# Kernel optimization log

Measured on AMD Instinct MI355X. Metric: run time of the kernel, lower is better.

## Reference

```python
import jax, jax.numpy as jnp
import numpy as np


def setup_inputs() -> dict:
    key = jax.random.key(0)
    k1, k2 = jax.random.split(key)
    x = jax.random.normal(k1, (2048, 512, 7, 7), dtype=jnp.float32)   # backbone feature map [B, C, H, W]
    db = jax.random.normal(k2, (50000, 512), dtype=jnp.float32)       # gallery embeddings [N, D]
    return {"x": x, "db": db}


def reference(x, db):
    # backbone output is a 4D feature map -> global average pool over H, W
    emb = x.mean(axis=(2, 3))                      # [B, 512]; width == 512 so no pad/slice
    # torch.cdist(emb, db, p=2) via ||a||^2 - 2ab + ||b||^2 decomposition
    a2 = jnp.sum(emb * emb, axis=1, keepdims=True)         # [B, 1]
    b2 = jnp.sum(db * db, axis=1)                          # [N]
    d2 = a2 - 2.0 * (emb @ db.T) + b2[None, :]             # [B, N]
    dist = jnp.sqrt(jnp.maximum(d2, 0.0))
    min_dist = jnp.min(dist, axis=1)                       # [B]
    min_idx = jnp.argmin(dist, axis=1)                     # [B] int
    return min_dist, min_idx
```

## Files before the change

kernel.cpp:

```cpp
#include <hip/hip_runtime.h>
#include <math.h>
#include <stdint.h>

#define D      512
#define K2T    1056
#define HW     49
#define BM     128
#define BN     128
#define BK     32
#define NSWEEP 4
#define KSTEPS 33
#define TTOT   (NSWEEP * KSTEPS)

typedef __attribute__((ext_vector_type(8))) _Float16 f16x8;
typedef __attribute__((ext_vector_type(4))) float f32x4;
typedef __attribute__((address_space(3))) uint32_t lds_t;
typedef const __attribute__((address_space(1))) uint32_t glb_t;

__global__ __launch_bounds__(256) void gap_split_kernel(const float* __restrict__ x,
                                                        _Float16* __restrict__ emb2) {
    __shared__ float g[256 * HW];
    const int tid = threadIdx.x;
    const float4* x4 = (const float4*)x + (size_t)blockIdx.x * (256 * HW / 4);
    float4* g4 = (float4*)g;
#pragma unroll
    for (int i = 0; i < 12; ++i) {
        g4[tid + i * 256] = x4[tid + i * 256];
    }
    if (tid < 64) g4[tid + 3072] = x4[tid + 3072];
    __syncthreads();
    const float* p = g + tid * HW;
    float s = 0.f;
#pragma unroll
    for (int j = 0; j < HW; ++j) s += p[j];
    s *= (1.f / 49.f);
    _Float16 hi = (_Float16)s;
    _Float16 lo = (_Float16)(s - (float)hi);
    int r = blockIdx.x * 256 + tid;
    int m = r >> 9, c = r & 511;
    emb2[(size_t)m * K2T + c]       = hi;
    emb2[(size_t)m * K2T + 512 + c] = lo;
}

__global__ void finishA_kernel(_Float16* __restrict__ emb2, int M) {
    int row = blockIdx.x * 4 + (threadIdx.x >> 6);
    if (row >= M) return;
    int lane = threadIdx.x & 63;
    _Float16* p = emb2 + (size_t)row * K2T;
    f16x8 h = *(const f16x8*)(p + lane * 8);
    f16x8 l = *(const f16x8*)(p + 512 + lane * 8);
    float s = 0.f;
#pragma unroll
    for (int i = 0; i < 8; ++i) { float v = (float)h[i] + (float)l[i]; s = fmaf(v, v, s); }
#pragma unroll
    for (int m2 = 32; m2; m2 >>= 1) s += __shfl_xor(s, m2, 64);
    if (lane == 0) {
        _Float16 a2h = (_Float16)s;
        _Float16 a2l = (_Float16)(s - (float)a2h);
        _Float16 one = (_Float16)1.f, z0 = (_Float16)0.f;
        f16x8 t0 = {one, one, a2h, a2l, z0, z0, z0, z0};
        f16x8 z  = {z0, z0, z0, z0, z0, z0, z0, z0};
        *(f16x8*)(p + 1024) = t0;
        *(f16x8*)(p + 1032) = z;
        *(f16x8*)(p + 1040) = z;
        *(f16x8*)(p + 1048) = z;
    }
}

__global__ void split_db_kernel(const float* __restrict__ db,
                                _Float16* __restrict__ db2, int N, int N2) {
    int row = blockIdx.x * 4 + (threadIdx.x >> 6);
    if (row >= N2) return;
    int lane = threadIdx.x & 63;
    _Float16* q = db2 + (size_t)row * K2T;
    _Float16 z0 = (_Float16)0.f;
    f16x8 z = {z0, z0, z0, z0, z0, z0, z0, z0};
    if (row < N) {
        const float* p = db + (size_t)row * D + lane * 8;
        float4 v0 = *(const float4*)p;
        float4 v1 = *(const float4*)(p + 4);
        float vv[8] = {v0.x, v0.y, v0.z, v0.w, v1.x, v1.y, v1.z, v1.w};
        f16x8 h, l;
        float s = 0.f;
#pragma unroll
        for (int i = 0; i < 8; ++i) {
            float v = vv[i];
            s = fmaf(v, v, s);
            float wv = -2.f * v;
            _Float16 hh = (_Float16)wv;
            h[i] = hh;
            l[i] = (_Float16)(wv - (float)hh);
        }
        *(f16x8*)(q + lane * 8)       = h;
        *(f16x8*)(q + 512 + lane * 8) = l;
#pragma unroll
        for (int m2 = 32; m2; m2 >>= 1) s += __shfl_xor(s, m2, 64);
        if (lane == 0) {
            _Float16 b2h = (_Float16)s;
            _Float16 b2l = (_Float16)(s - (float)b2h);
            _Float16 one = (_Float16)1.f;
            f16x8 t0 = {b2h, b2l, one, one, z0, z0, z0, z0};
            *(f16x8*)(q + 1024) = t0;
            *(f16x8*)(q + 1032) = z;
            *(f16x8*)(q + 1040) = z;
            *(f16x8*)(q + 1048) = z;
        }
    } else {
        *(f16x8*)(q + lane * 8)       = z;
        *(f16x8*)(q + 512 + lane * 8) = z;
        if (lane < 4) *(f16x8*)(q + 1024 + lane * 8) = z;
    }
}

__global__ void init_keys_kernel(unsigned long long* __restrict__ keys, int M) {
    int b = blockIdx.x * blockDim.x + threadIdx.x;
    if (b < M) keys[b] = ~0ull;
}

__global__ __launch_bounds__(256) void dist_kernel(
        const _Float16* __restrict__ A2, const _Float16* __restrict__ B2,
        unsigned long long* __restrict__ keys, int N, int nXcdChunk)
{
    __shared__ _Float16 lds[3 * 8192];
    const int tid  = threadIdx.x;
    const int lane = tid & 63;
    const int w    = tid >> 6;
    const int wr   = w >> 1, wc = w & 1;
    const int l15  = lane & 15, lg = lane >> 4;

    const int bb   = blockIdx.x;
    const int swz  = (bb & 7) * nXcdChunk + (bb >> 3);
    const int mBase = (swz & 15) * BM;
    const long long nSuperBase = (long long)(swz >> 4) * (BN * NSWEEP);

    const int o0 = w * 1024 + lane * 16;

    auto STAGE = [&](unsigned bufByte, int tt) {
        const int k0 = (tt % KSTEPS) * BK;
        const long long nB = nSuperBase + (long long)(tt / KSTEPS) * BN;
#pragma unroll
        for (int q = 0; q < 2; ++q) {
            const int o = o0 + q * 4096;
            const int row = o >> 6;
            const int slot = (o >> 4) & 3;
            const int cb = ((slot ^ ((row >> 1) & 3)) << 4);
            const char* ga = (const char*)A2 + ((size_t)(mBase + row) * K2T + k0) * 2 + cb;
            const char* gb = (const char*)B2 + ((size_t)(nB + row) * K2T + k0) * 2 + cb;
            char* la = (char*)lds + bufByte + q * 4096 + w * 1024;
            __builtin_amdgcn_global_load_lds((glb_t*)ga, (lds_t*)la, 16, 0, 0);
            __builtin_amdgcn_global_load_lds((glb_t*)gb, (lds_t*)(la + 8192), 16, 0, 0);
        }
    };

    unsigned long long key[4][4];
#pragma unroll
    for (int mF = 0; mF < 4; ++mF)
#pragma unroll
        for (int r = 0; r < 4; ++r) key[mF][r] = ~0ull;

    f32x4 acc[4][4];
#pragma unroll
    for (int mF = 0; mF < 4; ++mF)
#pragma unroll
        for (int nF = 0; nF < 4; ++nF) acc[mF][nF] = (f32x4){0.f, 0.f, 0.f, 0.f};

    STAGE(0, 0);
    STAGE(16384, 1);
    unsigned bufR = 0, bufN = 16384, bufP = 32768;

    const int sw = (lg ^ ((l15 >> 1) & 3)) * 8;

    for (int t = 0; t < TTOT; ++t) {
        if (t < TTOT - 1) asm volatile("s_waitcnt vmcnt(4)" ::: "memory");
        else              asm volatile("s_waitcnt vmcnt(0)" ::: "memory");
        __builtin_amdgcn_s_barrier();

        const _Float16* As = (const _Float16*)((const char*)lds + bufR);
        const _Float16* Bs = As + 4096;
        f16x8 af[4], bf[4];
#pragma unroll
        for (int mF = 0; mF < 4; ++mF)
            af[mF] = *(const f16x8*)(As + (wr * 64 + mF * 16 + l15) * BK + sw);
#pragma unroll
        for (int nF = 0; nF < 4; ++nF)
            bf[nF] = *(const f16x8*)(Bs + (wc * 64 + nF * 16 + l15) * BK + sw);

        if (t + 2 < TTOT) STAGE(bufP, t + 2);

        __builtin_amdgcn_s_setprio(1);
#pragma unroll
        for (int mF = 0; mF < 4; ++mF)
#pragma unroll
            for (int nF = 0; nF < 4; ++nF)
                acc[mF][nF] = __builtin_amdgcn_mfma_f32_16x16x32_f16(
                    af[mF], bf[nF], acc[mF][nF], 0, 0, 0);
        __builtin_amdgcn_s_setprio(0);

        if (t % KSTEPS == KSTEPS - 1) {
            const long long nBase = nSuperBase + (long long)(t / KSTEPS) * BN;
#pragma unroll
            for (int nF = 0; nF < 4; ++nF) {
                const long long g = nBase + wc * 64 + nF * 16 + l15;
                if (g < N) {
#pragma unroll
                    for (int mF = 0; mF < 4; ++mF)
#pragma unroll
                        for (int r = 0; r < 4; ++r) {
                            float d2 = fmaxf(acc[mF][nF][r], 0.f);
                            unsigned long long kk =
                                ((unsigned long long)__float_as_uint(d2) << 32) |
                                (unsigned long long)(unsigned)g;
                            key[mF][r] = key[mF][r] < kk ? key[mF][r] : kk;
                        }
                }
            }
#pragma unroll
            for (int mF = 0; mF < 4; ++mF)
#pragma unroll
                for (int nF = 0; nF < 4; ++nF) acc[mF][nF] = (f32x4){0.f, 0.f, 0.f, 0.f};
        }

        unsigned tmp = bufR; bufR = bufN; bufN = bufP; bufP = tmp;
    }

#pragma unroll
    for (int mF = 0; mF < 4; ++mF)
#pragma unroll
        for (int r = 0; r < 4; ++r) {
            unsigned long long k = key[mF][r];
#pragma unroll
            for (int m2 = 1; m2 < 16; m2 <<= 1) {
                unsigned long long o = __shfl_xor(k, m2, 16);
                k = k < o ? k : o;
            }
            if (l15 == 0)
                atomicMin(&keys[mBase + wr * 64 + mF * 16 + lg * 4 + r], k);
        }
}

__global__ void finalize_kernel(const unsigned long long* __restrict__ keys,
                                float* __restrict__ out_dist, float* __restrict__ out_idx, int M) {
    int b = blockIdx.x * blockDim.x + threadIdx.x;
    if (b >= M) return;
    unsigned long long k = keys[b];
    float d2 = __uint_as_float((unsigned)(k >> 32));
    out_dist[b] = sqrtf(fmaxf(d2, 0.f));
    out_idx[b]  = (float)(unsigned)(k & 0xffffffffu);
}

extern "C" void kernel_launch(void* const* d_in, const int* in_sizes, int n_in,
                              void* d_out, int out_size, void* d_ws, size_t ws_size,
                              hipStream_t stream) {
    const float* x  = (const float*)d_in[0];
    const float* db = (const float*)d_in[1];
    float* out = (float*)d_out;

    const int M  = in_sizes[0] / (D * HW);
    const int N  = in_sizes[1] / D;
    const int nTiles  = (N + BN - 1) / BN;
    const int nSupers = (nTiles + NSWEEP - 1) / NSWEEP;
    const int N2 = nSupers * NSWEEP * BN;
    const int mTiles = M / BM;
    const int nBlocks = nSupers * mTiles;
    const int nXcdChunk = nBlocks / 8;

    char* ws = (char*)d_ws;
    _Float16* emb2 = (_Float16*)ws;
    _Float16* db2  = emb2 + (size_t)M * K2T;
    unsigned long long* keys =
        (unsigned long long*)(((uintptr_t)(db2 + (size_t)N2 * K2T) + 7) & ~(uintptr_t)7);

    const int rows = M * D;
    gap_split_kernel<<<rows / 256, 256, 0, stream>>>(x, emb2);
    finishA_kernel<<<(M + 3) / 4, 256, 0, stream>>>(emb2, M);
    split_db_kernel<<<(N2 + 3) / 4, 256, 0, stream>>>(db, db2, N, N2);
    init_keys_kernel<<<(M + 255) / 256, 256, 0, stream>>>(keys, M);

    dist_kernel<<<nBlocks, 256, 0, stream>>>(emb2, db2, keys, N, nXcdChunk);

    finalize_kernel<<<(M + 255) / 256, 256, 0, stream>>>(keys, out, out + M, M);
}
```

Measured before the change: 657.4 us.

## Restructure distance GEMM into 256x256 tiles with 8 waves and split-phase pipelining

```diff
diff --git a/kernel.cpp b/kernel.cpp
--- a/kernel.cpp
+++ b/kernel.cpp
@@ -3,14 +3,11 @@
 #include <stdint.h>
 
 #define D      512
-#define K2T    1056
+#define K2T    1088
 #define HW     49
-#define BM     128
-#define BN     128
-#define BK     32
-#define NSWEEP 4
-#define KSTEPS 33
-#define TTOT   (NSWEEP * KSTEPS)
+#define BM     256
+#define BN     256
+#define KTILES 17
 
 typedef __attribute__((ext_vector_type(8))) _Float16 f16x8;
 typedef __attribute__((ext_vector_type(4))) float f32x4;
@@ -24,9 +21,7 @@
     const float4* x4 = (const float4*)x + (size_t)blockIdx.x * (256 * HW / 4);
     float4* g4 = (float4*)g;
 #pragma unroll
-    for (int i = 0; i < 12; ++i) {
-        g4[tid + i * 256] = x4[tid + i * 256];
-    }
+    for (int i = 0; i < 12; ++i) g4[tid + i * 256] = x4[tid + i * 256];
     if (tid < 64) g4[tid + 3072] = x4[tid + 3072];
     __syncthreads();
     const float* p = g + tid * HW;
@@ -61,9 +56,8 @@
         f16x8 t0 = {one, one, a2h, a2l, z0, z0, z0, z0};
         f16x8 z  = {z0, z0, z0, z0, z0, z0, z0, z0};
         *(f16x8*)(p + 1024) = t0;
-        *(f16x8*)(p + 1032) = z;
-        *(f16x8*)(p + 1040) = z;
-        *(f16x8*)(p + 1048) = z;
+#pragma unroll
+        for (int q = 1; q < 8; ++q) *(f16x8*)(p + 1024 + q * 8) = z;
     }
 }
 
@@ -101,14 +95,13 @@
             _Float16 one = (_Float16)1.f;
             f16x8 t0 = {b2h, b2l, one, one, z0, z0, z0, z0};
             *(f16x8*)(q + 1024) = t0;
-            *(f16x8*)(q + 1032) = z;
-            *(f16x8*)(q + 1040) = z;
-            *(f16x8*)(q + 1048) = z;
+#pragma unroll
+            for (int q2 = 1; q2 < 8; ++q2) *(f16x8*)(q + 1024 + q2 * 8) = z;
         }
     } else {
         *(f16x8*)(q + lane * 8)       = z;
         *(f16x8*)(q + 512 + lane * 8) = z;
-        if (lane < 4) *(f16x8*)(q + 1024 + lane * 8) = z;
+        if (lane < 8) *(f16x8*)(q + 1024 + lane * 8) = z;
     }
 }
 
@@ -117,125 +110,191 @@
     if (b < M) keys[b] = ~0ull;
 }
 
-__global__ __launch_bounds__(256) void dist_kernel(
+__global__ __launch_bounds__(512, 2) void dist_kernel(
         const _Float16* __restrict__ A2, const _Float16* __restrict__ B2,
         unsigned long long* __restrict__ keys, int N, int nXcdChunk)
 {
-    __shared__ _Float16 lds[3 * 8192];
+    __shared__ f16x8 ldsv[8192];
+    char* ldsb = (char*)ldsv;
     const int tid  = threadIdx.x;
     const int lane = tid & 63;
     const int w    = tid >> 6;
-    const int wr   = w >> 1, wc = w & 1;
+    const int wr   = w >> 2, wc = w & 3;
     const int l15  = lane & 15, lg = lane >> 4;
 
     const int bb   = blockIdx.x;
-    const int swz  = (bb & 7) * nXcdChunk + (bb >> 3);
-    const int mBase = (swz & 15) * BM;
-    const long long nSuperBase = (long long)(swz >> 4) * (BN * NSWEEP);
-
-    const int o0 = w * 1024 + lane * 16;
-
-    auto STAGE = [&](unsigned bufByte, int tt) {
-        const int k0 = (tt % KSTEPS) * BK;
-        const long long nB = nSuperBase + (long long)(tt / KSTEPS) * BN;
-#pragma unroll
-        for (int q = 0; q < 2; ++q) {
-            const int o = o0 + q * 4096;
-            const int row = o >> 6;
-            const int slot = (o >> 4) & 3;
-            const int cb = ((slot ^ ((row >> 1) & 3)) << 4);
-            const char* ga = (const char*)A2 + ((size_t)(mBase + row) * K2T + k0) * 2 + cb;
-            const char* gb = (const char*)B2 + ((size_t)(nB + row) * K2T + k0) * 2 + cb;
-            char* la = (char*)lds + bufByte + q * 4096 + w * 1024;
-            __builtin_amdgcn_global_load_lds((glb_t*)ga, (lds_t*)la, 16, 0, 0);
-            __builtin_amdgcn_global_load_lds((glb_t*)gb, (lds_t*)(la + 8192), 16, 0, 0);
+    const int swzb = (bb & 7) * nXcdChunk + (bb >> 3);
+    const long long mBase = (long long)(swzb & 7) * BM;
+    const long long nBase = (long long)(swzb >> 3) * BN;
+
+    auto STAGE_A = [&](int s2, int h, int tile) {
+#pragma unroll
+        for (int pass = 0; pass < 2; ++pass) {
+            const int o  = pass * 8192 + tid * 16;
+            const int rl = o >> 7;
+            const int sl = (o >> 4) & 7;
+            const int r  = h * 128 + rl;
+            const _Float16* g = A2 + (size_t)(mBase + r) * K2T + tile * 64 + ((sl ^ (r & 7)) << 3);
+            char* lp = ldsb + s2 * 65536 + h * 16384 + pass * 8192 + w * 1024;
+            __builtin_amdgcn_global_load_lds((glb_t*)g, (lds_t*)lp, 16, 0, 0);
         }
     };
-
-    unsigned long long key[4][4];
-#pragma unroll
-    for (int mF = 0; mF < 4; ++mF)
-#pragma unroll
-        for (int r = 0; r < 4; ++r) key[mF][r] = ~0ull;
-
-    f32x4 acc[4][4];
-#pragma unroll
-    for (int mF = 0; mF < 4; ++mF)
+    auto STAGE_B = [&](int s2, int h, int tile) {
+#pragma unroll
+        for (int pass = 0; pass < 2; ++pass) {
+            const int o  = pass * 8192 + tid * 16;
+            const int rl = o >> 7;
+            const int sl = (o >> 4) & 7;
+            const int r  = h * 128 + rl;
+            const _Float16* g = B2 + (size_t)(nBase + r) * K2T + tile * 64 + ((sl ^ (r & 7)) << 3);
+            char* lp = ldsb + s2 * 65536 + 32768 + h * 16384 + pass * 8192 + w * 1024;
+            __builtin_amdgcn_global_load_lds((glb_t*)g, (lds_t*)lp, 16, 0, 0);
+        }
+    };
+
+    f32x4 acc[8][4];
+#pragma unroll
+    for (int mF = 0; mF < 8; ++mF)
 #pragma unroll
         for (int nF = 0; nF < 4; ++nF) acc[mF][nF] = (f32x4){0.f, 0.f, 0.f, 0.f};
-
-    STAGE(0, 0);
-    STAGE(16384, 1);
-    unsigned bufR = 0, bufN = 16384, bufP = 32768;
-
-    const int sw = (lg ^ ((l15 >> 1) & 3)) * 8;
-
-    for (int t = 0; t < TTOT; ++t) {
-        if (t < TTOT - 1) asm volatile("s_waitcnt vmcnt(4)" ::: "memory");
-        else              asm volatile("s_waitcnt vmcnt(0)" ::: "memory");
-        __builtin_amdgcn_s_barrier();
-
-        const _Float16* As = (const _Float16*)((const char*)lds + bufR);
-        const _Float16* Bs = As + 4096;
-        f16x8 af[4], bf[4];
-#pragma unroll
-        for (int mF = 0; mF < 4; ++mF)
-            af[mF] = *(const f16x8*)(As + (wr * 64 + mF * 16 + l15) * BK + sw);
+    f16x8 bf[4][2], af[2][2];
+
+    STAGE_A(0, 0, 0); STAGE_A(0, 1, 0);
+    STAGE_B(0, 0, 0); STAGE_B(0, 1, 0);
+    STAGE_B(1, 0, 1); STAGE_B(1, 1, 1);
+
+    for (int t = 0; t < KTILES; ++t) {
+        const int s  = t & 1;
+        const int sA = s * 65536;
+        const int sB = sA + 32768;
+
+        if (t < KTILES - 1) asm volatile("s_waitcnt vmcnt(4)" ::: "memory");
+        else                asm volatile("s_waitcnt vmcnt(0)" ::: "memory");
+        __builtin_amdgcn_s_barrier();
 #pragma unroll
         for (int nF = 0; nF < 4; ++nF)
-            bf[nF] = *(const f16x8*)(Bs + (wc * 64 + nF * 16 + l15) * BK + sw);
-
-        if (t + 2 < TTOT) STAGE(bufP, t + 2);
-
+#pragma unroll
+            for (int kk = 0; kk < 2; ++kk) {
+                const int r = wc * 64 + nF * 16 + l15;
+                bf[nF][kk] = *(const f16x8*)(ldsb + sB + r * 128 + (((kk << 2) | lg) ^ (r & 7)) * 16);
+            }
+#pragma unroll
+        for (int j = 0; j < 2; ++j)
+#pragma unroll
+            for (int kk = 0; kk < 2; ++kk) {
+                const int r = wr * 128 + (0 + j) * 16 + l15;
+                af[j][kk] = *(const f16x8*)(ldsb + sA + r * 128 + (((kk << 2) | lg) ^ (r & 7)) * 16);
+            }
+        if (t + 1 < KTILES) STAGE_A(s ^ 1, 0, t + 1);
+        __builtin_amdgcn_s_barrier();
+        asm volatile("s_waitcnt lgkmcnt(0)" ::: "memory");
         __builtin_amdgcn_s_setprio(1);
 #pragma unroll
-        for (int mF = 0; mF < 4; ++mF)
+        for (int j = 0; j < 2; ++j)
 #pragma unroll
             for (int nF = 0; nF < 4; ++nF)
-                acc[mF][nF] = __builtin_amdgcn_mfma_f32_16x16x32_f16(
-                    af[mF], bf[nF], acc[mF][nF], 0, 0, 0);
+#pragma unroll
+                for (int kk = 0; kk < 2; ++kk)
+                    acc[0 + j][nF] = __builtin_amdgcn_mfma_f32_16x16x32_f16(af[j][kk], bf[nF][kk], acc[0 + j][nF], 0, 0, 0);
         __builtin_amdgcn_s_setprio(0);
-
-        if (t % KSTEPS == KSTEPS - 1) {
-            const long long nBase = nSuperBase + (long long)(t / KSTEPS) * BN;
+        __builtin_amdgcn_s_barrier();
+
+#pragma unroll
+        for (int j = 0; j < 2; ++j)
+#pragma unroll
+            for (int kk = 0; kk < 2; ++kk) {
+                const int r = wr * 128 + (2 + j) * 16 + l15;
+                af[j][kk] = *(const f16x8*)(ldsb + sA + r * 128 + (((kk << 2) | lg) ^ (r & 7)) * 16);
+            }
+        if (t + 1 < KTILES) STAGE_A(s ^ 1, 1, t + 1);
+        if (t + 2 < KTILES) STAGE_B(s, 0, t + 2);
+        __builtin_amdgcn_s_barrier();
+        asm volatile("s_waitcnt lgkmcnt(0)" ::: "memory");
+        __builtin_amdgcn_s_setprio(1);
+#pragma unroll
+        for (int j = 0; j < 2; ++j)
+#pragma unroll
+            for (int nF = 0; nF < 4; ++nF)
+#pragma unroll
+                for (int kk = 0; kk < 2; ++kk)
+                    acc[2 + j][nF] = __builtin_amdgcn_mfma_f32_16x16x32_f16(af[j][kk], bf[nF][kk], acc[2 + j][nF], 0, 0, 0);
+        __builtin_amdgcn_s_setprio(0);
+        __builtin_amdgcn_s_barrier();
+
+#pragma unroll
+        for (int j = 0; j < 2; ++j)
+#pragma unroll
+            for (int kk = 0; kk < 2; ++kk) {
+                const int r = wr * 128 + (4 + j) * 16 + l15;
+                af[j][kk] = *(const f16x8*)(ldsb + sA + r * 128 + (((kk << 2) | lg) ^ (r & 7)) * 16);
+            }
+        if (t + 2 < KTILES) STAGE_B(s, 1, t + 2);
+        __builtin_amdgcn_s_barrier();
+        asm volatile("s_waitcnt lgkmcnt(0)" ::: "memory");
+        __builtin_amdgcn_s_setprio(1);
+#pragma unroll
+        for (int j = 0; j < 2; ++j)
+#pragma unroll
+            for (int nF = 0; nF < 4; ++nF)
+#pragma unroll
+                for (int kk = 0; kk < 2; ++kk)
+                    acc[4 + j][nF] = __builtin_amdgcn_mfma_f32_16x16x32_f16(af[j][kk], bf[nF][kk], acc[4 + j][nF], 0, 0, 0);
+        __builtin_amdgcn_s_setprio(0);
+        __builtin_amdgcn_s_barrier();
+
+#pragma unroll
+        for (int j = 0; j < 2; ++j)
+#pragma unroll
+            for (int kk = 0; kk < 2; ++kk) {
+                const int r = wr * 128 + (6 + j) * 16 + l15;
+                af[j][kk] = *(const f16x8*)(ldsb + sA + r * 128 + (((kk << 2) | lg) ^ (r & 7)) * 16);
+            }
+        __builtin_amdgcn_s_barrier();
+        asm volatile("s_waitcnt lgkmcnt(0)" ::: "memory");
+        __builtin_amdgcn_s_setprio(1);
+#pragma unroll
+        for (int j = 0; j < 2; ++j)
+#pragma unroll
+            for (int nF = 0; nF < 4; ++nF)
+#pragma unroll
+                for (int kk = 0; kk < 2; ++kk)
+                    acc[6 + j][nF] = __builtin_amdgcn_mfma_f32_16x16x32_f16(af[j][kk], bf[nF][kk], acc[6 + j][nF], 0, 0, 0);
+        __builtin_amdgcn_s_setprio(0);
+    }
+
+    unsigned long long* ldsK = (unsigned long long*)ldsv;
+#pragma unroll
+    for (int mF = 0; mF < 8; ++mF)
+#pragma unroll
+        for (int r = 0; r < 4; ++r) {
+            unsigned long long k = ~0ull;
 #pragma unroll
             for (int nF = 0; nF < 4; ++nF) {
                 const long long g = nBase + wc * 64 + nF * 16 + l15;
                 if (g < N) {
-#pragma unroll
-                    for (int mF = 0; mF < 4; ++mF)
-#pragma unroll
-                        for (int r = 0; r < 4; ++r) {
-                            float d2 = fmaxf(acc[mF][nF][r], 0.f);
-                            unsigned long long kk =
-                                ((unsigned long long)__float_as_uint(d2) << 32) |
-                                (unsigned long long)(unsigned)g;
-                            key[mF][r] = key[mF][r] < kk ? key[mF][r] : kk;
-                        }
+                    float d2 = fmaxf(acc[mF][nF][r], 0.f);
+                    unsigned long long kk2 =
+                        ((unsigned long long)__float_as_uint(d2) << 32) | (unsigned long long)(unsigned)g;
+                    k = k < kk2 ? k : kk2;
                 }
             }
-#pragma unroll
-            for (int mF = 0; mF < 4; ++mF)
-#pragma unroll
-                for (int nF = 0; nF < 4; ++nF) acc[mF][nF] = (f32x4){0.f, 0.f, 0.f, 0.f};
-        }
-
-        unsigned tmp = bufR; bufR = bufN; bufN = bufP; bufP = tmp;
-    }
-
-#pragma unroll
-    for (int mF = 0; mF < 4; ++mF)
-#pragma unroll
-        for (int r = 0; r < 4; ++r) {
-            unsigned long long k = key[mF][r];
 #pragma unroll
             for (int m2 = 1; m2 < 16; m2 <<= 1) {
                 unsigned long long o = __shfl_xor(k, m2, 16);
                 k = k < o ? k : o;
             }
-            if (l15 == 0)
-                atomicMin(&keys[mBase + wr * 64 + mF * 16 + lg * 4 + r], k);
-        }
+            if (l15 == 0) ldsK[(wr * 128 + mF * 16 + lg * 4 + r) * 4 + wc] = k;
+        }
+    __syncthreads();
+    if (tid < 256) {
+        unsigned long long k = ldsK[tid * 4 + 0];
+#pragma unroll
+        for (int q = 1; q < 4; ++q) {
+            unsigned long long o = ldsK[tid * 4 + q];
+            k = k < o ? k : o;
+        }
+        atomicMin(&keys[mBase + tid], k);
+    }
 }
 
 __global__ void finalize_kernel(const unsigned long long* __restrict__ keys,
@@ -257,11 +316,10 @@
 
     const int M  = in_sizes[0] / (D * HW);
     const int N  = in_sizes[1] / D;
-    const int nTiles  = (N + BN - 1) / BN;
-    const int nSupers = (nTiles + NSWEEP - 1) / NSWEEP;
-    const int N2 = nSupers * NSWEEP * BN;
+    const int nTiles = (N + BN - 1) / BN;
+    const int N2 = nTiles * BN;
     const int mTiles = M / BM;
-    const int nBlocks = nSupers * mTiles;
+    const int nBlocks = mTiles * nTiles;
     const int nXcdChunk = nBlocks / 8;
 
     char* ws = (char*)d_ws;
@@ -276,7 +334,7 @@
     split_db_kernel<<<(N2 + 3) / 4, 256, 0, stream>>>(db, db2, N, N2);
     init_keys_kernel<<<(M + 255) / 256, 256, 0, stream>>>(keys, M);
 
-    dist_kernel<<<nBlocks, 256, 0, stream>>>(emb2, db2, keys, N, nXcdChunk);
+    dist_kernel<<<nBlocks, 512, 0, stream>>>(emb2, db2, keys, N, nXcdChunk);
 
     finalize_kernel<<<(M + 255) / 256, 256, 0, stream>>>(keys, out, out + M, M);
 }
```

New measurement: 618.2 us. 6.0% less time.
